# Kernel optimization log

Measured on AMD Instinct MI355X. Metric: run time of the kernel, lower is better.

The kernel has to match this reference:

```python
import jax, jax.numpy as jnp
import numpy as np
from jax import lax

N = 40       # num_users
K = 20       # num_channels
F = 3        # num_features (conv length dim)
SS = K * N   # state_size = 800
B = 16384


def _conv1d(x, w, b):
    # x: [B, C_in, L], w: [C_out, C_in, 3], SAME padding (pad=1)
    y = lax.conv_general_dilated(x, w, window_strides=(1,), padding=[(1, 1)],
                                 dimension_numbers=('NCH', 'OIH', 'NCH'))
    return y + b[None, :, None]


def _get_mask(state):
    # state: [B, SS, F]; status feature is index 2 (== -1 since F=3)
    visited = state[:, :, 2] != 0.0                      # [B, SS]
    vm = visited.reshape(B, K, N)                        # [B, K, N] (flat idx = chan*N + user)
    user_any = vm.any(axis=1)                            # [B, N]: user visited on any channel
    chan_full = vm.sum(axis=2) >= 2                      # [B, K]: channel has >=2 users
    mask = visited \
        | jnp.broadcast_to(user_any[:, None, :], (B, K, N)).reshape(B, SS) \
        | jnp.broadcast_to(chan_full[:, :, None], (B, K, N)).reshape(B, SS)
    return mask


def setup_inputs() -> dict:
    key = jax.random.key(0)
    ks = jax.random.split(key, 12)
    state = jax.random.normal(ks[0], (B, SS, F), jnp.float32)
    keep = jax.random.bernoulli(ks[1], 0.02, (B, SS)).astype(jnp.float32)
    state = state.at[:, :, 2].multiply(keep)
    s = 0.02
    w1 = jax.random.normal(ks[2], (128, SS, 3), jnp.float32) * s
    b1 = jnp.zeros((128,), jnp.float32)
    w2 = jax.random.normal(ks[3], (256, 128, 3), jnp.float32) * s
    b2 = jnp.zeros((256,), jnp.float32)
    w3 = jax.random.normal(ks[4], (128, 256, 3), jnp.float32) * s
    b3 = jnp.zeros((128,), jnp.float32)
    wl1 = jax.random.normal(ks[5], (64 * F, 128 * F), jnp.float32) * s   # [192, 384]
    bl1 = jnp.zeros((64 * F,), jnp.float32)
    wl2 = jax.random.normal(ks[6], (SS, 64 * F), jnp.float32) * s        # [800, 192]
    bl2 = jnp.zeros((SS,), jnp.float32)
    return {"state": state, "w1": w1, "b1": b1, "w2": w2, "b2": b2,
            "w3": w3, "b3": b3, "wl1": wl1, "bl1": bl1, "wl2": wl2, "bl2": bl2}


def reference(state, w1, b1, w2, b2, w3, b3, wl1, bl1, wl2, bl2):
    mask = _get_mask(state)
    x = jax.nn.relu(_conv1d(state, w1, b1))   # [B,128,3]
    x = jax.nn.relu(_conv1d(x, w2, b2))       # [B,256,3]
    x = jax.nn.relu(_conv1d(x, w3, b3))       # [B,128,3]
    x = x.reshape(B, -1)                      # [B,384]
    x = jax.nn.relu(x @ wl1.T + bl1)          # [B,192]
    out = x @ wl2.T + bl2                     # [B,800]
    return jnp.where(mask, -jnp.inf, out)
```

## Files before the change

kernel.cpp:

```cpp
#include <hip/hip_runtime.h>
#include <cstdint>
#include <cstddef>
#include <math.h>

typedef short bf16x8 __attribute__((ext_vector_type(8)));
typedef float f32x4 __attribute__((ext_vector_type(4)));
typedef unsigned long long u64;

#define NEG_HUGE (-3.0e38f)

__device__ __forceinline__ ushort f2bf(float x) {
    union { float f; uint32_t u; } a; a.f = x;
    uint32_t r = a.u + 0x7FFF + ((a.u >> 16) & 1);
    return (ushort)(r >> 16);
}

__global__ void prep_conv_T(const float* __restrict__ w, ushort* __restrict__ WT,
                            int Cin, int Cout, int Nrows, int Kpad) {
    int idx = blockIdx.x * 256 + threadIdx.x;
    if (idx >= Nrows * Kpad) return;
    int n = idx / Kpad, k = idx - n * Kpad;
    float val = 0.f;
    if (k < Cin * 3) {
        int co = n / 3, l = n % 3, ci = k / 3, lx = k % 3;
        int t = lx - l + 1;
        if (t >= 0 && t < 3) val = w[(co * Cin + ci) * 3 + t];
    }
    WT[idx] = f2bf(val);
}

__global__ void prep_lin_T(const float* __restrict__ wl, ushort* __restrict__ WT,
                           int K, int Nreal, int Npad) {
    int idx = blockIdx.x * 256 + threadIdx.x;
    if (idx >= Npad * K) return;
    int n = idx / K, k = idx - n * K;
    WT[idx] = (n < Nreal) ? f2bf(wl[n * K + k]) : (ushort)0;
}

#define SPB 64
#define LDS_X1   0
#define LDS_X2   49152
#define LDS_MASK 147456
#define LDS_TOTAL 153856

template<int NF, int MF, int KSTEPS, int LDX>
__device__ __forceinline__ void layer_mfma(const char* xlds,
                                           const ushort* __restrict__ WT, int ldw,
                                           int wn0, int mbase, int lane,
                                           f32x4 (&acc)[NF][MF]) {
    const int ml = lane & 15, kq = lane >> 4;
    #pragma unroll 4
    for (int ks = 0; ks < KSTEPS; ++ks) {
        bf16x8 af[NF];
        #pragma unroll
        for (int f = 0; f < NF; ++f)
            af[f] = *(const bf16x8*)(WT + (size_t)(wn0 + f * 16 + ml) * ldw + ks * 32 + kq * 8);
        bf16x8 bv[MF];
        #pragma unroll
        for (int mi = 0; mi < MF; ++mi) {
            int m = mbase + mi * 16 + ml;
            bv[mi] = *(const bf16x8*)(xlds + m * LDX + ((((ks * 4 + kq) * 16)) ^ ((m & 7) << 4)));
        }
        #pragma unroll
        for (int f = 0; f < NF; ++f)
            #pragma unroll
            for (int mi = 0; mi < MF; ++mi)
                acc[f][mi] = __builtin_amdgcn_mfma_f32_16x16x32_bf16(af[f], bv[mi], acc[f][mi], 0, 0, 0);
    }
}

template<int NF, int MF, bool RELU, bool BDIV3>
__device__ __forceinline__ void epi_lds(f32x4 (&acc)[NF][MF], char* xout, int ldo,
                                        const float* __restrict__ bias,
                                        int wn0, int mbase, int lane) {
    const int ml = lane & 15, nq4 = (lane >> 4) * 4;
    #pragma unroll
    for (int f = 0; f < NF; ++f) {
        const int n4 = wn0 + f * 16 + nq4;
        float bv[4];
        #pragma unroll
        for (int r = 0; r < 4; ++r) bv[r] = bias[BDIV3 ? (n4 + r) / 3 : (n4 + r)];
        #pragma unroll
        for (int mi = 0; mi < MF; ++mi) {
            int m = mbase + mi * 16 + ml;
            ushort4 o;
            float x0 = acc[f][mi][0] + bv[0];
            float x1 = acc[f][mi][1] + bv[1];
            float x2 = acc[f][mi][2] + bv[2];
            float x3 = acc[f][mi][3] + bv[3];
            if (RELU) { x0 = fmaxf(x0, 0.f); x1 = fmaxf(x1, 0.f);
                        x2 = fmaxf(x2, 0.f); x3 = fmaxf(x3, 0.f); }
            o.x = f2bf(x0); o.y = f2bf(x1); o.z = f2bf(x2); o.w = f2bf(x3);
            *(ushort4*)(xout + m * ldo + ((n4 * 2) ^ ((m & 7) << 4))) = o;
        }
    }
}

__global__ __launch_bounds__(512, 2)
void fused_net(const float* __restrict__ state,
               const ushort* __restrict__ W1T, const float* __restrict__ b1,
               const ushort* __restrict__ W2T, const float* __restrict__ b2,
               const ushort* __restrict__ W3T, const float* __restrict__ b3,
               const ushort* __restrict__ WL1T, const float* __restrict__ bl1,
               const ushort* __restrict__ WL2T, const float* __restrict__ bl2,
               float* __restrict__ out)
{
    extern __shared__ char lds[];
    const int tid = threadIdx.x;
    const int lane = tid & 63, wid = tid >> 6;
    const int m0 = blockIdx.x * SPB;
    uint32_t* maskw = (uint32_t*)(lds + LDS_MASK);
    char* stg = lds + LDS_X2;

    for (int i = tid; i < SPB * 25; i += 512) maskw[i] = 0;

    const int sr = tid >> 3, seg = tid & 7;
    const float* srow = state + (size_t)(m0 + sr) * 2400 + seg * 16;
    const int wn1 = wid * 48;

    f32x4 acc1[3][4];
    #pragma unroll
    for (int f = 0; f < 3; ++f)
        #pragma unroll
        for (int mi = 0; mi < 4; ++mi) acc1[f][mi] = (f32x4){0.f, 0.f, 0.f, 0.f};

    float4 svA[4], svB[4];
    auto loadc = [&](float4 (&sv)[4], int c) {
        int kb = c * 128 + seg * 16;
        if (kb <= 2384) {
            #pragma unroll
            for (int q = 0; q < 4; ++q) sv[q] = *(const float4*)(srow + c * 128 + q * 4);
        } else {
            #pragma unroll
            for (int q = 0; q < 4; ++q) sv[q] = (float4){0.f, 0.f, 0.f, 0.f};
        }
    };
    auto stage_write = [&](float4 (&sv)[4], int c) {
        int kbase = c * 128 + seg * 16;
        float fv[16] = {sv[0].x, sv[0].y, sv[0].z, sv[0].w,
                        sv[1].x, sv[1].y, sv[1].z, sv[1].w,
                        sv[2].x, sv[2].y, sv[2].z, sv[2].w,
                        sv[3].x, sv[3].y, sv[3].z, sv[3].w};
        bf16x8 h0, h1;
        #pragma unroll
        for (int j = 0; j < 8; ++j) h0[j] = (short)f2bf(fv[j]);
        #pragma unroll
        for (int j = 0; j < 8; ++j) h1[j] = (short)f2bf(fv[8 + j]);
        const int rb = sr * 256, xo = (sr & 7) << 4;
        *(bf16x8*)(stg + rb + ((seg * 32) ^ xo)) = h0;
        *(bf16x8*)(stg + rb + ((seg * 32 + 16) ^ xo)) = h1;
        int kmod = kbase % 3;
        uint32_t* mrow = maskw + sr * 25;
        #define MCHK(J) { if (fv[J] != 0.0f) { int a = (kbase + (J)) / 3; \
                          atomicOr(&mrow[a >> 5], 1u << (a & 31)); } }
        if (kmod == 0)      { MCHK(2) MCHK(5) MCHK(8) MCHK(11) MCHK(14) }
        else if (kmod == 1) { MCHK(1) MCHK(4) MCHK(7) MCHK(10) MCHK(13) }
        else                { MCHK(0) MCHK(3) MCHK(6) MCHK(9) MCHK(12) MCHK(15) }
        #undef MCHK
    };

    loadc(svA, 0);
    loadc(svB, 1);
    __syncthreads();

    #define C1STEP(SV, C, CN) \
        stage_write(SV, C); \
        __syncthreads(); \
        if ((CN) <= 18) loadc(SV, CN); \
        layer_mfma<3, 4, 4, 256>(stg, W1T + (C) * 128, 2432, wn1, 0, lane, acc1); \
        __syncthreads();

    for (int p = 0; p < 9; ++p) {
        int c0 = 2 * p;
        C1STEP(svA, c0, c0 + 2)
        C1STEP(svB, c0 + 1, c0 + 3)
    }
    C1STEP(svA, 18, 99)
    #undef C1STEP

    epi_lds<3, 4, true, true>(acc1, lds + LDS_X1, 768, b1, wn1, 0, lane);

    if (tid < SPB) {
        uint32_t* mw = maskw + tid * 25;
        const u64 M40 = (1ull << 40) - 1;
        u64 ua = 0; uint32_t cf = 0;
        #pragma unroll
        for (int g = 0; g < 5; ++g) {
            uint32_t w0 = mw[5*g], w1 = mw[5*g+1], w2 = mw[5*g+2], w3 = mw[5*g+3], w4 = mw[5*g+4];
            u64 c0 = ( (u64)w0        | ((u64)w1 << 32)) & M40;
            u64 c1 = (((u64)w1 >> 8)  | ((u64)w2 << 24)) & M40;
            u64 c2 = (((u64)w2 >> 16) | ((u64)w3 << 16)) & M40;
            u64 c3 = (((u64)w3 >> 24) | ((u64)w4 << 8))  & M40;
            ua |= c0 | c1 | c2 | c3;
            if (__popcll(c0) >= 2) cf |= 1u << (4*g);
            if (__popcll(c1) >= 2) cf |= 1u << (4*g+1);
            if (__popcll(c2) >= 2) cf |= 1u << (4*g+2);
            if (__popcll(c3) >= 2) cf |= 1u << (4*g+3);
        }
        #pragma unroll
        for (int g = 0; g < 5; ++g) {
            uint32_t w0 = mw[5*g], w1 = mw[5*g+1], w2 = mw[5*g+2], w3 = mw[5*g+3], w4 = mw[5*g+4];
            u64 c0 = ( (u64)w0        | ((u64)w1 << 32)) & M40;
            u64 c1 = (((u64)w1 >> 8)  | ((u64)w2 << 24)) & M40;
            u64 c2 = (((u64)w2 >> 16) | ((u64)w3 << 16)) & M40;
            u64 c3 = (((u64)w3 >> 24) | ((u64)w4 << 8))  & M40;
            u64 m0v = c0 | ua | (((cf >> (4*g))     & 1u) ? M40 : 0ull);
            u64 m1v = c1 | ua | (((cf >> (4*g + 1)) & 1u) ? M40 : 0ull);
            u64 m2v = c2 | ua | (((cf >> (4*g + 2)) & 1u) ? M40 : 0ull);
            u64 m3v = c3 | ua | (((cf >> (4*g + 3)) & 1u) ? M40 : 0ull);
            mw[5*g]   = (uint32_t)m0v;
            mw[5*g+1] = (uint32_t)(m0v >> 32) | (uint32_t)(m1v << 8);
            mw[5*g+2] = (uint32_t)(m1v >> 24) | (uint32_t)(m2v << 16);
            mw[5*g+3] = (uint32_t)(m2v >> 16) | (uint32_t)(m3v << 24);
            mw[5*g+4] = (uint32_t)(m3v >> 8);
        }
    }
    __syncthreads();

    f32x4 acc2[6][4];
    #pragma unroll
    for (int f = 0; f < 6; ++f)
        #pragma unroll
        for (int mi = 0; mi < 4; ++mi) acc2[f][mi] = (f32x4){0.f, 0.f, 0.f, 0.f};
    layer_mfma<6, 4, 12, 768>(lds + LDS_X1, W2T, 384, wid * 96, 0, lane, acc2);
    epi_lds<6, 4, true, true>(acc2, lds + LDS_X2, 1536, b2, wid * 96, 0, lane);
    __syncthreads();

    f32x4 acc3[3][4];
    #pragma unroll
    for (int f = 0; f < 3; ++f)
        #pragma unroll
        for (int mi = 0; mi < 4; ++mi) acc3[f][mi] = (f32x4){0.f, 0.f, 0.f, 0.f};
    layer_mfma<3, 4, 24, 1536>(lds + LDS_X2, W3T, 768, wid * 48, 0, lane, acc3);
    epi_lds<3, 4, true, true>(acc3, lds + LDS_X1, 768, b3, wid * 48, 0, lane);
    __syncthreads();

    const int mh = wid >> 2, nq = wid & 3;
    f32x4 acc4[3][2];
    #pragma unroll
    for (int f = 0; f < 3; ++f)
        #pragma unroll
        for (int mi = 0; mi < 2; ++mi) acc4[f][mi] = (f32x4){0.f, 0.f, 0.f, 0.f};
    layer_mfma<3, 2, 12, 768>(lds + LDS_X1, WL1T, 384, nq * 48, mh * 32, lane, acc4);
    epi_lds<3, 2, true, false>(acc4, lds + LDS_X2, 384, bl1, nq * 48, mh * 32, lane);
    __syncthreads();

    f32x4 acc5[7][4];
    #pragma unroll
    for (int f = 0; f < 7; ++f)
        #pragma unroll
        for (int mi = 0; mi < 4; ++mi) acc5[f][mi] = (f32x4){0.f, 0.f, 0.f, 0.f};
    layer_mfma<7, 4, 6, 384>(lds + LDS_X2, WL2T, 192, wid * 112, 0, lane, acc5);
    {
        const int ml = lane & 15, nq4 = (lane >> 4) * 4;
        #pragma unroll
        for (int f = 0; f < 7; ++f) {
            int nf = wid * 112 + f * 16;
            if (nf < 800) {
                int n4 = nf + nq4, sh = n4 & 31;
                float bv0 = bl2[n4], bv1 = bl2[n4 + 1], bv2 = bl2[n4 + 2], bv3 = bl2[n4 + 3];
                #pragma unroll
                for (int mi = 0; mi < 4; ++mi) {
                    int m = mi * 16 + ml;
                    uint32_t mwv = maskw[m * 25 + (nf >> 5)];
                    float4 v;
                    v.x = ((mwv >> (sh + 0)) & 1u) ? NEG_HUGE : (acc5[f][mi][0] + bv0);
                    v.y = ((mwv >> (sh + 1)) & 1u) ? NEG_HUGE : (acc5[f][mi][1] + bv1);
                    v.z = ((mwv >> (sh + 2)) & 1u) ? NEG_HUGE : (acc5[f][mi][2] + bv2);
                    v.w = ((mwv >> (sh + 3)) & 1u) ? NEG_HUGE : (acc5[f][mi][3] + bv3);
                    *(float4*)(out + (size_t)(m0 + m) * 800 + n4) = v;
                }
            }
        }
    }
}

__global__ void ws_fail_kernel(float* out) {
    if (threadIdx.x == 0 && blockIdx.x == 0) out[0] = NAN;
}

extern "C" void kernel_launch(void* const* d_in, const int* in_sizes, int n_in,
                              void* d_out, int out_size, void* d_ws, size_t ws_size,
                              hipStream_t stream) {
    const float* state = (const float*)d_in[0];
    const float* w1  = (const float*)d_in[1];
    const float* b1  = (const float*)d_in[2];
    const float* w2  = (const float*)d_in[3];
    const float* b2  = (const float*)d_in[4];
    const float* w3  = (const float*)d_in[5];
    const float* b3  = (const float*)d_in[6];
    const float* wl1 = (const float*)d_in[7];
    const float* bl1 = (const float*)d_in[8];
    const float* wl2 = (const float*)d_in[9];
    const float* bl2 = (const float*)d_in[10];
    float* out = (float*)d_out;

    char* ws = (char*)d_ws;
    size_t off = 0;
    auto carve = [&](size_t bytes) {
        char* p = ws + off;
        off = (off + bytes + 255) & ~(size_t)255;
        return p;
    };
    ushort* W1T  = (ushort*)carve(384ull * 2432 * 2);
    ushort* W2T  = (ushort*)carve(768ull * 384 * 2);
    ushort* W3T  = (ushort*)carve(384ull * 768 * 2);
    ushort* WL1T = (ushort*)carve(192ull * 384 * 2);
    ushort* WL2T = (ushort*)carve(896ull * 192 * 2);

    if (off > ws_size) {
        ws_fail_kernel<<<1, 64, 0, stream>>>(out);
        return;
    }

    prep_conv_T<<<(384 * 2432 + 255) / 256, 256, 0, stream>>>(w1, W1T, 800, 128, 384, 2432);
    prep_conv_T<<<(768 * 384 + 255) / 256, 256, 0, stream>>>(w2, W2T, 128, 256, 768, 384);
    prep_conv_T<<<(384 * 768 + 255) / 256, 256, 0, stream>>>(w3, W3T, 256, 128, 384, 768);
    prep_lin_T<<<(192 * 384 + 255) / 256, 256, 0, stream>>>(wl1, WL1T, 384, 192, 192);
    prep_lin_T<<<(896 * 192 + 255) / 256, 256, 0, stream>>>(wl2, WL2T, 192, 800, 896);

    hipFuncSetAttribute(reinterpret_cast<const void*>(fused_net),
                        hipFuncAttributeMaxDynamicSharedMemorySize, LDS_TOTAL);
    fused_net<<<256, 512, LDS_TOTAL, stream>>>(state, W1T, b1, W2T, b2, W3T, b3,
                                               WL1T, bl1, WL2T, bl2, out);
}
```

Before: 165.5 us.

## Split fused network into per-layer tiled GEMM kernels with async LDS loads

Replaces the single fused kernel that ran all five layers per 64-row block with a pipeline of separate kernels. A pre-pass converts the state to bf16 in global memory and builds the action mask. A templated GEMM kernel then double-buffers A and W tiles into LDS with global_load_lds and is launched once per layer with a 2D grid. This gives more blocks, better occupancy and LDS-staged weights, but intermediate activations now round-trip through global memory, there are extra launches, and a full bf16 copy of the input is written and re-read.

```diff
diff --git a/kernel.cpp b/kernel.cpp
--- a/kernel.cpp
+++ b/kernel.cpp
@@ -14,6 +14,17 @@
     uint32_t r = a.u + 0x7FFF + ((a.u >> 16) & 1);
     return (ushort)(r >> 16);
 }
+
+__device__ __forceinline__ void gload_lds16(const void* g, void* l) {
+    __builtin_amdgcn_global_load_lds(
+        (const __attribute__((address_space(1))) uint32_t*)g,
+        (__attribute__((address_space(3))) uint32_t*)l, 16, 0, 0);
+}
+
+#define VMCNT0() asm volatile("s_waitcnt vmcnt(0)" ::: "memory")
+#define SBAR() do { __builtin_amdgcn_sched_barrier(0); \
+    __builtin_amdgcn_s_barrier(); \
+    __builtin_amdgcn_sched_barrier(0); } while (0)
 
 __global__ void prep_conv_T(const float* __restrict__ w, ushort* __restrict__ WT,
                             int Cin, int Cout, int Nrows, int Kpad) {
@@ -37,238 +48,203 @@
     WT[idx] = (n < Nreal) ? f2bf(wl[n * K + k]) : (ushort)0;
 }
 
-#define SPB 64
-#define LDS_X1   0
-#define LDS_X2   49152
-#define LDS_MASK 147456
-#define LDS_TOTAL 153856
-
-template<int NF, int MF, int KSTEPS, int LDX>
-__device__ __forceinline__ void layer_mfma(const char* xlds,
-                                           const ushort* __restrict__ WT, int ldw,
-                                           int wn0, int mbase, int lane,
-                                           f32x4 (&acc)[NF][MF]) {
+__global__ void zero_mask(uint32_t* __restrict__ maskg) {
+    int i = blockIdx.x * 256 + threadIdx.x;
+    if (i < 16384 * 25) maskg[i] = 0;
+}
+
+__global__ void convert_kernel(const float* __restrict__ state, ushort* __restrict__ Abf,
+                               uint32_t* __restrict__ maskg) {
+    int gid = blockIdx.x * 256 + threadIdx.x;
+    if (gid >= 16384 * 304) return;
+    int row = gid / 304, t = gid - row * 304;
+    ushort* dst = Abf + (size_t)row * 2432 + t * 8;
+    if (t >= 300) {
+        *(uint4*)dst = (uint4){0, 0, 0, 0};
+        return;
+    }
+    const float* src = state + (size_t)row * 2400 + t * 8;
+    float4 a = *(const float4*)src, b = *(const float4*)(src + 4);
+    float fv[8] = {a.x, a.y, a.z, a.w, b.x, b.y, b.z, b.w};
+    ushort4 h0 = {f2bf(fv[0]), f2bf(fv[1]), f2bf(fv[2]), f2bf(fv[3])};
+    ushort4 h1 = {f2bf(fv[4]), f2bf(fv[5]), f2bf(fv[6]), f2bf(fv[7])};
+    *(ushort4*)dst = h0;
+    *(ushort4*)(dst + 4) = h1;
+    int k0 = t * 8;
+    int j0 = (2 - (k0 % 3) + 3) % 3;
+    #pragma unroll
+    for (int j = 0; j < 8; ++j) {
+        if (((j - j0) % 3) == 0 && j >= j0) {
+            if (fv[j] != 0.0f) {
+                int aidx = (k0 + j) / 3;
+                atomicOr(&maskg[row * 25 + (aidx >> 5)], 1u << (aidx & 31));
+            }
+        }
+    }
+}
+
+__global__ void mask_finalize(uint32_t* __restrict__ maskg) {
+    int row = blockIdx.x * 256 + threadIdx.x;
+    if (row >= 16384) return;
+    uint32_t* mw = maskg + (size_t)row * 25;
+    uint32_t w[25];
+    #pragma unroll
+    for (int i = 0; i < 25; ++i) w[i] = mw[i];
+    const u64 M40 = (1ull << 40) - 1;
+    u64 ua = 0; uint32_t cf = 0;
+    #pragma unroll
+    for (int g = 0; g < 5; ++g) {
+        uint32_t w0 = w[5*g], w1 = w[5*g+1], w2 = w[5*g+2], w3 = w[5*g+3], w4 = w[5*g+4];
+        u64 c0 = ( (u64)w0        | ((u64)w1 << 32)) & M40;
+        u64 c1 = (((u64)w1 >> 8)  | ((u64)w2 << 24)) & M40;
+        u64 c2 = (((u64)w2 >> 16) | ((u64)w3 << 16)) & M40;
+        u64 c3 = (((u64)w3 >> 24) | ((u64)w4 << 8))  & M40;
+        ua |= c0 | c1 | c2 | c3;
+        if (__popcll(c0) >= 2) cf |= 1u << (4*g);
+        if (__popcll(c1) >= 2) cf |= 1u << (4*g+1);
+        if (__popcll(c2) >= 2) cf |= 1u << (4*g+2);
+        if (__popcll(c3) >= 2) cf |= 1u << (4*g+3);
+    }
+    #pragma unroll
+    for (int g = 0; g < 5; ++g) {
+        uint32_t w0 = w[5*g], w1 = w[5*g+1], w2 = w[5*g+2], w3 = w[5*g+3], w4 = w[5*g+4];
+        u64 c0 = ( (u64)w0        | ((u64)w1 << 32)) & M40;
+        u64 c1 = (((u64)w1 >> 8)  | ((u64)w2 << 24)) & M40;
+        u64 c2 = (((u64)w2 >> 16) | ((u64)w3 << 16)) & M40;
+        u64 c3 = (((u64)w3 >> 24) | ((u64)w4 << 8))  & M40;
+        u64 m0v = c0 | ua | (((cf >> (4*g))     & 1u) ? M40 : 0ull);
+        u64 m1v = c1 | ua | (((cf >> (4*g + 1)) & 1u) ? M40 : 0ull);
+        u64 m2v = c2 | ua | (((cf >> (4*g + 2)) & 1u) ? M40 : 0ull);
+        u64 m3v = c3 | ua | (((cf >> (4*g + 3)) & 1u) ? M40 : 0ull);
+        mw[5*g]   = (uint32_t)m0v;
+        mw[5*g+1] = (uint32_t)(m0v >> 32) | (uint32_t)(m1v << 8);
+        mw[5*g+2] = (uint32_t)(m1v >> 24) | (uint32_t)(m2v << 16);
+        mw[5*g+3] = (uint32_t)(m2v >> 16) | (uint32_t)(m3v << 24);
+        mw[5*g+4] = (uint32_t)(m3v >> 8);
+    }
+}
+
+template<int K, int MF, int NF, int WM, int WN, bool BDIV3, bool RELU, bool F32OUT>
+__global__ __launch_bounds__(512, 4)
+void glayer2(const ushort* __restrict__ Ag, const ushort* __restrict__ WTg,
+             const float* __restrict__ bias, void* __restrict__ Yg, int ldy,
+             const uint32_t* __restrict__ maskg)
+{
+    constexpr int MT = WM * MF * 16;
+    constexpr int NT = WN * NF * 16;
+    constexpr int NC = K / 64;
+    constexpr int ABYTES = MT * 128;
+    constexpr int WBYTES = NT * 128;
+    constexpr int WSLOTS = NT * 8;
+    extern __shared__ char lds[];
+
+    const int tid = threadIdx.x, lane = tid & 63, wid = tid >> 6;
+    const int m0 = blockIdx.x * MT;
+    const int n0 = blockIdx.y * NT;
     const int ml = lane & 15, kq = lane >> 4;
-    #pragma unroll 4
-    for (int ks = 0; ks < KSTEPS; ++ks) {
-        bf16x8 af[NF];
-        #pragma unroll
-        for (int f = 0; f < NF; ++f)
-            af[f] = *(const bf16x8*)(WT + (size_t)(wn0 + f * 16 + ml) * ldw + ks * 32 + kq * 8);
-        bf16x8 bv[MF];
-        #pragma unroll
-        for (int mi = 0; mi < MF; ++mi) {
-            int m = mbase + mi * 16 + ml;
-            bv[mi] = *(const bf16x8*)(xlds + m * LDX + ((((ks * 4 + kq) * 16)) ^ ((m & 7) << 4)));
-        }
-        #pragma unroll
-        for (int f = 0; f < NF; ++f)
+    const int mw = wid / WN, nw = wid % WN;
+    const int mbase = mw * MF * 16;
+    const int wn0 = nw * NF * 16;
+
+    f32x4 acc[NF][MF];
+    #pragma unroll
+    for (int f = 0; f < NF; ++f)
+        #pragma unroll
+        for (int mi = 0; mi < MF; ++mi) acc[f][mi] = (f32x4){0.f, 0.f, 0.f, 0.f};
+
+    auto stage = [&](int c, int b) {
+        char* Ab = lds + b * ABYTES;
+        char* Wb = lds + 2 * ABYTES + b * WBYTES;
+        {
+            int r = tid >> 3, o8 = tid & 7;
+            gload_lds16(Ag + (size_t)(m0 + r) * K + c * 64 + ((o8 ^ (r & 7)) * 8),
+                        Ab + tid * 16);
+        }
+        #pragma unroll
+        for (int i = 0; i < (WSLOTS + 511) / 512; ++i) {
+            int s = i * 512 + tid;
+            if ((WSLOTS % 512 == 0) || s < WSLOTS) {
+                int r = s >> 3, o8 = s & 7;
+                gload_lds16(WTg + (size_t)(n0 + r) * K + c * 64 + ((o8 ^ (r & 7)) * 8),
+                            Wb + s * 16);
+            }
+        }
+    };
+    auto mfmaC = [&](int b) {
+        const char* Ab = lds + b * ABYTES;
+        const char* Wb = lds + 2 * ABYTES + b * WBYTES;
+        #pragma unroll
+        for (int ks = 0; ks < 2; ++ks) {
+            bf16x8 af[NF], bv[MF];
             #pragma unroll
-            for (int mi = 0; mi < MF; ++mi)
-                acc[f][mi] = __builtin_amdgcn_mfma_f32_16x16x32_bf16(af[f], bv[mi], acc[f][mi], 0, 0, 0);
-    }
-}
-
-template<int NF, int MF, bool RELU, bool BDIV3>
-__device__ __forceinline__ void epi_lds(f32x4 (&acc)[NF][MF], char* xout, int ldo,
-                                        const float* __restrict__ bias,
-                                        int wn0, int mbase, int lane) {
-    const int ml = lane & 15, nq4 = (lane >> 4) * 4;
-    #pragma unroll
-    for (int f = 0; f < NF; ++f) {
-        const int n4 = wn0 + f * 16 + nq4;
-        float bv[4];
-        #pragma unroll
-        for (int r = 0; r < 4; ++r) bv[r] = bias[BDIV3 ? (n4 + r) / 3 : (n4 + r)];
-        #pragma unroll
-        for (int mi = 0; mi < MF; ++mi) {
-            int m = mbase + mi * 16 + ml;
-            ushort4 o;
-            float x0 = acc[f][mi][0] + bv[0];
-            float x1 = acc[f][mi][1] + bv[1];
-            float x2 = acc[f][mi][2] + bv[2];
-            float x3 = acc[f][mi][3] + bv[3];
-            if (RELU) { x0 = fmaxf(x0, 0.f); x1 = fmaxf(x1, 0.f);
-                        x2 = fmaxf(x2, 0.f); x3 = fmaxf(x3, 0.f); }
-            o.x = f2bf(x0); o.y = f2bf(x1); o.z = f2bf(x2); o.w = f2bf(x3);
-            *(ushort4*)(xout + m * ldo + ((n4 * 2) ^ ((m & 7) << 4))) = o;
-        }
-    }
-}
-
-__global__ __launch_bounds__(512, 2)
-void fused_net(const float* __restrict__ state,
-               const ushort* __restrict__ W1T, const float* __restrict__ b1,
-               const ushort* __restrict__ W2T, const float* __restrict__ b2,
-               const ushort* __restrict__ W3T, const float* __restrict__ b3,
-               const ushort* __restrict__ WL1T, const float* __restrict__ bl1,
-               const ushort* __restrict__ WL2T, const float* __restrict__ bl2,
-               float* __restrict__ out)
-{
-    extern __shared__ char lds[];
-    const int tid = threadIdx.x;
-    const int lane = tid & 63, wid = tid >> 6;
-    const int m0 = blockIdx.x * SPB;
-    uint32_t* maskw = (uint32_t*)(lds + LDS_MASK);
-    char* stg = lds + LDS_X2;
-
-    for (int i = tid; i < SPB * 25; i += 512) maskw[i] = 0;
-
-    const int sr = tid >> 3, seg = tid & 7;
-    const float* srow = state + (size_t)(m0 + sr) * 2400 + seg * 16;
-    const int wn1 = wid * 48;
-
-    f32x4 acc1[3][4];
-    #pragma unroll
-    for (int f = 0; f < 3; ++f)
-        #pragma unroll
-        for (int mi = 0; mi < 4; ++mi) acc1[f][mi] = (f32x4){0.f, 0.f, 0.f, 0.f};
-
-    float4 svA[4], svB[4];
-    auto loadc = [&](float4 (&sv)[4], int c) {
-        int kb = c * 128 + seg * 16;
-        if (kb <= 2384) {
+            for (int f = 0; f < NF; ++f) {
+                int n = wn0 + f * 16 + ml;
+                af[f] = *(const bf16x8*)(Wb + n * 128 + (((ks * 4 + kq) * 16) ^ ((n & 7) << 4)));
+            }
             #pragma unroll
-            for (int q = 0; q < 4; ++q) sv[q] = *(const float4*)(srow + c * 128 + q * 4);
-        } else {
+            for (int mi = 0; mi < MF; ++mi) {
+                int m = mbase + mi * 16 + ml;
+                bv[mi] = *(const bf16x8*)(Ab + m * 128 + (((ks * 4 + kq) * 16) ^ ((m & 7) << 4)));
+            }
             #pragma unroll
-            for (int q = 0; q < 4; ++q) sv[q] = (float4){0.f, 0.f, 0.f, 0.f};
+            for (int f = 0; f < NF; ++f)
+                #pragma unroll
+                for (int mi = 0; mi < MF; ++mi)
+                    acc[f][mi] = __builtin_amdgcn_mfma_f32_16x16x32_bf16(af[f], bv[mi], acc[f][mi], 0, 0, 0);
         }
     };
-    auto stage_write = [&](float4 (&sv)[4], int c) {
-        int kbase = c * 128 + seg * 16;
-        float fv[16] = {sv[0].x, sv[0].y, sv[0].z, sv[0].w,
-                        sv[1].x, sv[1].y, sv[1].z, sv[1].w,
-                        sv[2].x, sv[2].y, sv[2].z, sv[2].w,
-                        sv[3].x, sv[3].y, sv[3].z, sv[3].w};
-        bf16x8 h0, h1;
-        #pragma unroll
-        for (int j = 0; j < 8; ++j) h0[j] = (short)f2bf(fv[j]);
-        #pragma unroll
-        for (int j = 0; j < 8; ++j) h1[j] = (short)f2bf(fv[8 + j]);
-        const int rb = sr * 256, xo = (sr & 7) << 4;
-        *(bf16x8*)(stg + rb + ((seg * 32) ^ xo)) = h0;
-        *(bf16x8*)(stg + rb + ((seg * 32 + 16) ^ xo)) = h1;
-        int kmod = kbase % 3;
-        uint32_t* mrow = maskw + sr * 25;
-        #define MCHK(J) { if (fv[J] != 0.0f) { int a = (kbase + (J)) / 3; \
-                          atomicOr(&mrow[a >> 5], 1u << (a & 31)); } }
-        if (kmod == 0)      { MCHK(2) MCHK(5) MCHK(8) MCHK(11) MCHK(14) }
-        else if (kmod == 1) { MCHK(1) MCHK(4) MCHK(7) MCHK(10) MCHK(13) }
-        else                { MCHK(0) MCHK(3) MCHK(6) MCHK(9) MCHK(12) MCHK(15) }
-        #undef MCHK
-    };
-
-    loadc(svA, 0);
-    loadc(svB, 1);
-    __syncthreads();
-
-    #define C1STEP(SV, C, CN) \
-        stage_write(SV, C); \
-        __syncthreads(); \
-        if ((CN) <= 18) loadc(SV, CN); \
-        layer_mfma<3, 4, 4, 256>(stg, W1T + (C) * 128, 2432, wn1, 0, lane, acc1); \
-        __syncthreads();
-
-    for (int p = 0; p < 9; ++p) {
-        int c0 = 2 * p;
-        C1STEP(svA, c0, c0 + 2)
-        C1STEP(svB, c0 + 1, c0 + 3)
-    }
-    C1STEP(svA, 18, 99)
-    #undef C1STEP
-
-    epi_lds<3, 4, true, true>(acc1, lds + LDS_X1, 768, b1, wn1, 0, lane);
-
-    if (tid < SPB) {
-        uint32_t* mw = maskw + tid * 25;
-        const u64 M40 = (1ull << 40) - 1;
-        u64 ua = 0; uint32_t cf = 0;
-        #pragma unroll
-        for (int g = 0; g < 5; ++g) {
-            uint32_t w0 = mw[5*g], w1 = mw[5*g+1], w2 = mw[5*g+2], w3 = mw[5*g+3], w4 = mw[5*g+4];
-            u64 c0 = ( (u64)w0        | ((u64)w1 << 32)) & M40;
-            u64 c1 = (((u64)w1 >> 8)  | ((u64)w2 << 24)) & M40;
-            u64 c2 = (((u64)w2 >> 16) | ((u64)w3 << 16)) & M40;
-            u64 c3 = (((u64)w3 >> 24) | ((u64)w4 << 8))  & M40;
-            ua |= c0 | c1 | c2 | c3;
-            if (__popcll(c0) >= 2) cf |= 1u << (4*g);
-            if (__popcll(c1) >= 2) cf |= 1u << (4*g+1);
-            if (__popcll(c2) >= 2) cf |= 1u << (4*g+2);
-            if (__popcll(c3) >= 2) cf |= 1u << (4*g+3);
-        }
-        #pragma unroll
-        for (int g = 0; g < 5; ++g) {
-            uint32_t w0 = mw[5*g], w1 = mw[5*g+1], w2 = mw[5*g+2], w3 = mw[5*g+3], w4 = mw[5*g+4];
-            u64 c0 = ( (u64)w0        | ((u64)w1 << 32)) & M40;
-            u64 c1 = (((u64)w1 >> 8)  | ((u64)w2 << 24)) & M40;
-            u64 c2 = (((u64)w2 >> 16) | ((u64)w3 << 16)) & M40;
-            u64 c3 = (((u64)w3 >> 24) | ((u64)w4 << 8))  & M40;
-            u64 m0v = c0 | ua | (((cf >> (4*g))     & 1u) ? M40 : 0ull);
-            u64 m1v = c1 | ua | (((cf >> (4*g + 1)) & 1u) ? M40 : 0ull);
-            u64 m2v = c2 | ua | (((cf >> (4*g + 2)) & 1u) ? M40 : 0ull);
-            u64 m3v = c3 | ua | (((cf >> (4*g + 3)) & 1u) ? M40 : 0ull);
-            mw[5*g]   = (uint32_t)m0v;
-            mw[5*g+1] = (uint32_t)(m0v >> 32) | (uint32_t)(m1v << 8);
-            mw[5*g+2] = (uint32_t)(m1v >> 24) | (uint32_t)(m2v << 16);
-            mw[5*g+3] = (uint32_t)(m2v >> 16) | (uint32_t)(m3v << 24);
-            mw[5*g+4] = (uint32_t)(m3v >> 8);
-        }
-    }
-    __syncthreads();
-
-    f32x4 acc2[6][4];
-    #pragma unroll
-    for (int f = 0; f < 6; ++f)
-        #pragma unroll
-        for (int mi = 0; mi < 4; ++mi) acc2[f][mi] = (f32x4){0.f, 0.f, 0.f, 0.f};
-    layer_mfma<6, 4, 12, 768>(lds + LDS_X1, W2T, 384, wid * 96, 0, lane, acc2);
-    epi_lds<6, 4, true, true>(acc2, lds + LDS_X2, 1536, b2, wid * 96, 0, lane);
-    __syncthreads();
-
-    f32x4 acc3[3][4];
-    #pragma unroll
-    for (int f = 0; f < 3; ++f)
-        #pragma unroll
-        for (int mi = 0; mi < 4; ++mi) acc3[f][mi] = (f32x4){0.f, 0.f, 0.f, 0.f};
-    layer_mfma<3, 4, 24, 1536>(lds + LDS_X2, W3T, 768, wid * 48, 0, lane, acc3);
-    epi_lds<3, 4, true, true>(acc3, lds + LDS_X1, 768, b3, wid * 48, 0, lane);
-    __syncthreads();
-
-    const int mh = wid >> 2, nq = wid & 3;
-    f32x4 acc4[3][2];
-    #pragma unroll
-    for (int f = 0; f < 3; ++f)
-        #pragma unroll
-        for (int mi = 0; mi < 2; ++mi) acc4[f][mi] = (f32x4){0.f, 0.f, 0.f, 0.f};
-    layer_mfma<3, 2, 12, 768>(lds + LDS_X1, WL1T, 384, nq * 48, mh * 32, lane, acc4);
-    epi_lds<3, 2, true, false>(acc4, lds + LDS_X2, 384, bl1, nq * 48, mh * 32, lane);
-    __syncthreads();
-
-    f32x4 acc5[7][4];
-    #pragma unroll
-    for (int f = 0; f < 7; ++f)
-        #pragma unroll
-        for (int mi = 0; mi < 4; ++mi) acc5[f][mi] = (f32x4){0.f, 0.f, 0.f, 0.f};
-    layer_mfma<7, 4, 6, 384>(lds + LDS_X2, WL2T, 192, wid * 112, 0, lane, acc5);
-    {
-        const int ml = lane & 15, nq4 = (lane >> 4) * 4;
-        #pragma unroll
-        for (int f = 0; f < 7; ++f) {
-            int nf = wid * 112 + f * 16;
+
+    stage(0, 0);
+    VMCNT0();
+    SBAR();
+
+    #pragma unroll 1
+    for (int c = 0; c < NC; ++c) {
+        if (c + 1 < NC) stage(c + 1, (c + 1) & 1);
+        mfmaC(c & 1);
+        if (c + 1 < NC) { VMCNT0(); SBAR(); }
+    }
+
+    const int nq4 = (lane >> 4) * 4;
+    if (!F32OUT) {
+        ushort* Y = (ushort*)Yg;
+        #pragma unroll
+        for (int f = 0; f < NF; ++f) {
+            int n4 = n0 + wn0 + f * 16 + nq4;
+            float bv0 = bias[BDIV3 ? n4 / 3 : n4];
+            float bv1 = bias[BDIV3 ? (n4 + 1) / 3 : n4 + 1];
+            float bv2 = bias[BDIV3 ? (n4 + 2) / 3 : n4 + 2];
+            float bv3 = bias[BDIV3 ? (n4 + 3) / 3 : n4 + 3];
+            #pragma unroll
+            for (int mi = 0; mi < MF; ++mi) {
+                int m = mbase + mi * 16 + ml;
+                float x0 = acc[f][mi][0] + bv0, x1 = acc[f][mi][1] + bv1;
+                float x2 = acc[f][mi][2] + bv2, x3 = acc[f][mi][3] + bv3;
+                if (RELU) { x0 = fmaxf(x0, 0.f); x1 = fmaxf(x1, 0.f);
+                            x2 = fmaxf(x2, 0.f); x3 = fmaxf(x3, 0.f); }
+                ushort4 o = {f2bf(x0), f2bf(x1), f2bf(x2), f2bf(x3)};
+                *(ushort4*)(Y + (size_t)(m0 + m) * ldy + n4) = o;
+            }
+        }
+    } else {
+        float* Y = (float*)Yg;
+        #pragma unroll
+        for (int f = 0; f < NF; ++f) {
+            int nf = n0 + wn0 + f * 16;
             if (nf < 800) {
                 int n4 = nf + nq4, sh = n4 & 31;
-                float bv0 = bl2[n4], bv1 = bl2[n4 + 1], bv2 = bl2[n4 + 2], bv3 = bl2[n4 + 3];
+                float bv0 = bias[n4], bv1 = bias[n4 + 1];
+                float bv2 = bias[n4 + 2], bv3 = bias[n4 + 3];
                 #pragma unroll
-                for (int mi = 0; mi < 4; ++mi) {
-                    int m = mi * 16 + ml;
-                    uint32_t mwv = maskw[m * 25 + (nf >> 5)];
+                for (int mi = 0; mi < MF; ++mi) {
+                    int m = mbase + mi * 16 + ml;
+                    uint32_t mwv = maskg[(size_t)(m0 + m) * 25 + (nf >> 5)];
                     float4 v;
-                    v.x = ((mwv >> (sh + 0)) & 1u) ? NEG_HUGE : (acc5[f][mi][0] + bv0);
-                    v.y = ((mwv >> (sh + 1)) & 1u) ? NEG_HUGE : (acc5[f][mi][1] + bv1);
-                    v.z = ((mwv >> (sh + 2)) & 1u) ? NEG_HUGE : (acc5[f][mi][2] + bv2);
-                    v.w = ((mwv >> (sh + 3)) & 1u) ? NEG_HUGE : (acc5[f][mi][3] + bv3);
-                    *(float4*)(out + (size_t)(m0 + m) * 800 + n4) = v;
+                    v.x = ((mwv >> (sh + 0)) & 1u) ? NEG_HUGE : (acc[f][mi][0] + bv0);
+                    v.y = ((mwv >> (sh + 1)) & 1u) ? NEG_HUGE : (acc[f][mi][1] + bv1);
+                    v.z = ((mwv >> (sh + 2)) & 1u) ? NEG_HUGE : (acc[f][mi][2] + bv2);
+                    v.w = ((mwv >> (sh + 3)) & 1u) ? NEG_HUGE : (acc[f][mi][3] + bv3);
+                    *(float4*)(Y + (size_t)(m0 + m) * ldy + n4) = v;
                 }
             }
         }
@@ -307,6 +283,12 @@
     ushort* W3T  = (ushort*)carve(384ull * 768 * 2);
     ushort* WL1T = (ushort*)carve(192ull * 384 * 2);
     ushort* WL2T = (ushort*)carve(896ull * 192 * 2);
+    ushort* Abf  = (ushort*)carve(16384ull * 2432 * 2);
+    ushort* X1g  = (ushort*)carve(16384ull * 384 * 2);
+    uint32_t* maskg = (uint32_t*)carve(16384ull * 25 * 4);
+    ushort* X2g = Abf;
+    ushort* X3g = (ushort*)((char*)Abf + (32ull << 20));
+    ushort* X4g = (ushort*)((char*)Abf + (48ull << 20));
 
     if (off > ws_size) {
         ws_fail_kernel<<<1, 64, 0, stream>>>(out);
@@ -319,8 +301,32 @@
     prep_lin_T<<<(192 * 384 + 255) / 256, 256, 0, stream>>>(wl1, WL1T, 384, 192, 192);
     prep_lin_T<<<(896 * 192 + 255) / 256, 256, 0, stream>>>(wl2, WL2T, 192, 800, 896);
 
-    hipFuncSetAttribute(reinterpret_cast<const void*>(fused_net),
-                        hipFuncAttributeMaxDynamicSharedMemorySize, LDS_TOTAL);
-    fused_net<<<256, 512, LDS_TOTAL, stream>>>(state, W1T, b1, W2T, b2, W3T, b3,
-                                               WL1T, bl1, WL2T, bl2, out);
-}
+    zero_mask<<<(16384 * 25 + 255) / 256, 256, 0, stream>>>(maskg);
+    convert_kernel<<<(16384 * 304 + 255) / 256, 256, 0, stream>>>(state, Abf, maskg);
+    mask_finalize<<<16384 / 256, 256, 0, stream>>>(maskg);
+
+    auto kc1 = glayer2<2432, 2, 3, 2, 4, true, true, false>;
+    (void)hipFuncSetAttribute(reinterpret_cast<const void*>(kc1),
+                        hipFuncAttributeMaxDynamicSharedMemorySize, 65536);
+    kc1<<<dim3(256, 2), 512, 65536, stream>>>(Abf, W1T, b1, X1g, 384, nullptr);
+
+    auto kc2 = glayer2<384, 2, 3, 2, 4, true, true, false>;
+    (void)hipFuncSetAttribute(reinterpret_cast<const void*>(kc2),
+                        hipFuncAttributeMaxDynamicSharedMemorySize, 65536);
+    kc2<<<dim3(256, 4), 512, 65536, stream>>>(X1g, W2T, b2, X2g, 768, nullptr);
+
+    auto kc3 = glayer2<768, 2, 3, 2, 4, true, true, false>;
+    (void)hipFuncSetAttribute(reinterpret_cast<const void*>(kc3),
+                        hipFuncAttributeMaxDynamicSharedMemorySize, 65536);
+    kc3<<<dim3(256, 2), 512, 65536, stream>>>(X2g, W3T, b3, X3g, 384, nullptr);
+
+    auto kc4 = glayer2<384, 2, 3, 2, 4, false, true, false>;
+    (void)hipFuncSetAttribute(reinterpret_cast<const void*>(kc4),
+                        hipFuncAttributeMaxDynamicSharedMemorySize, 65536);
+    kc4<<<dim3(256, 1), 512, 65536, stream>>>(X3g, WL1T, bl1, X4g, 192, nullptr);
+
+    auto kc5 = glayer2<192, 1, 7, 4, 2, false, false, true>;
+    (void)hipFuncSetAttribute(reinterpret_cast<const void*>(kc5),
+                        hipFuncAttributeMaxDynamicSharedMemorySize, 73728);
+    kc5<<<dim3(256, 4), 512, 73728, stream>>>(X4g, WL2T, bl2, out, 800, maskg);
+}
```

New measurement: 169.0 us. +2.2%, slower.
